# Kernel optimization log

Measured on AMD Instinct MI355X. Metric: run time of the kernel, lower is better.

## Reference

```python
import jax, jax.numpy as jnp
import numpy as np

D_MODEL = 1024
D_FF = 4096
N_HEADS = 16
D_HEAD = D_MODEL // N_HEADS
EPS = 1e-6


def setup_inputs() -> dict:
    key = jax.random.key(0)
    ks = jax.random.split(key, 12)
    B, S = 8, 1024
    s = 1.0 / np.sqrt(D_MODEL)
    inp = {
        "x": jax.random.normal(ks[0], (B, S, D_MODEL), dtype=jnp.float32),
        "mask": jnp.zeros((B, S, S), dtype=bool),
        "gamma1": jnp.ones((D_MODEL,), jnp.float32),
        "beta1": jnp.zeros((D_MODEL,), jnp.float32),
        "Wq": jax.random.normal(ks[1], (D_MODEL, D_MODEL), jnp.float32) * s,
        "bq": jnp.zeros((D_MODEL,), jnp.float32),
        "Wk": jax.random.normal(ks[2], (D_MODEL, D_MODEL), jnp.float32) * s,
        "bk": jnp.zeros((D_MODEL,), jnp.float32),
        "Wv": jax.random.normal(ks[3], (D_MODEL, D_MODEL), jnp.float32) * s,
        "bv": jnp.zeros((D_MODEL,), jnp.float32),
        "Wo": jax.random.normal(ks[4], (D_MODEL, D_MODEL), jnp.float32) * s,
        "bo": jnp.zeros((D_MODEL,), jnp.float32),
        "gamma2": jnp.ones((D_MODEL,), jnp.float32),
        "beta2": jnp.zeros((D_MODEL,), jnp.float32),
        "W1": jax.random.normal(ks[5], (D_MODEL, D_FF), jnp.float32) * s,
        "b1": jnp.zeros((D_FF,), jnp.float32),
        "W2": jax.random.normal(ks[6], (D_FF, D_MODEL), jnp.float32) * (1.0 / np.sqrt(D_FF)),
        "b2": jnp.zeros((D_MODEL,), jnp.float32),
    }
    return inp


def layer_norm(x, gamma, beta):
    mean = jnp.mean(x, axis=-1, keepdims=True)
    var = jnp.mean(jnp.square(x - mean), axis=-1, keepdims=True)  # unbiased=False
    return gamma * (x - mean) / jnp.sqrt(var + EPS) + beta


def mha(x, mask, Wq, bq, Wk, bk, Wv, bv, Wo, bo):
    B, S, _ = x.shape
    # projections: [B,S,D] -> [B,H,S,dh]
    q = (x @ Wq + bq).reshape(B, S, N_HEADS, D_HEAD).transpose(0, 2, 1, 3)
    k = (x @ Wk + bk).reshape(B, S, N_HEADS, D_HEAD).transpose(0, 2, 1, 3)
    v = (x @ Wv + bv).reshape(B, S, N_HEADS, D_HEAD).transpose(0, 2, 1, 3)
    # scores: [B,H,Sq,Sk]
    scores = jnp.einsum("bhqd,bhkd->bhqk", q, k) / np.sqrt(D_HEAD)
    scores = jnp.where(mask[:, None, :, :], -jnp.inf, scores)
    attn = jax.nn.softmax(scores, axis=-1)
    out = jnp.einsum("bhqk,bhkd->bhqd", attn, v)  # [B,H,Sq,dh]
    out = out.transpose(0, 2, 1, 3).reshape(B, S, D_MODEL)
    return out @ Wo + bo


def reference(x, mask, gamma1, beta1, Wq, bq, Wk, bk, Wv, bv, Wo, bo,
              gamma2, beta2, W1, b1, W2, b2):
    # pre-layer-norm variant per source: x = ln1(x); x = x + attn(x); x = ln2(x); x = x + ff(x)
    x = layer_norm(x, gamma1, beta1)
    x = x + mha(x, mask, Wq, bq, Wk, bk, Wv, bv, Wo, bo)
    x = layer_norm(x, gamma2, beta2)
    ff = jax.nn.relu(x @ W1 + b1) @ W2 + b2
    return x + ff
```

## Files before the change

### kernel.cpp

```cpp
#include <hip/hip_runtime.h>
#include <hip/hip_bf16.h>

typedef __bf16 bf16;
typedef __bf16 bf16x8 __attribute__((ext_vector_type(8)));
typedef __bf16 bf16x4 __attribute__((ext_vector_type(4)));
typedef float  f32x4  __attribute__((ext_vector_type(4)));

#define N_HEADS 16
#define D_HEAD  64
#define SEQ     1024
#define BATCH   8
#define MROWS   (BATCH * SEQ)

__device__ __forceinline__ void gld_lds16(const void* g, void* l) {
    __builtin_amdgcn_global_load_lds(
        (const __attribute__((address_space(1))) void*)g,
        (__attribute__((address_space(3))) void*)l, 16, 0, 0);
}

__global__ __launch_bounds__(256)
void wconv_t(const float* __restrict__ W, bf16* __restrict__ Wt, int K, int N)
{
    __shared__ float tile[32][33];
    const int tx = threadIdx.x & 31, ty = threadIdx.x >> 5;
    const int nb = blockIdx.x * 32, kb = blockIdx.y * 32;
    #pragma unroll
    for (int i = 0; i < 4; ++i)
        tile[ty + i * 8][tx] = W[(size_t)(kb + ty + i * 8) * N + nb + tx];
    __syncthreads();
    #pragma unroll
    for (int i = 0; i < 4; ++i)
        Wt[(size_t)(nb + ty + i * 8) * K + kb + tx] = (bf16)tile[tx][ty + i * 8];
}

__global__ __launch_bounds__(256)
void bconcat(const float* __restrict__ bq, const float* __restrict__ bk,
             const float* __restrict__ bv, float* __restrict__ o)
{
    const int i = blockIdx.x * 256 + threadIdx.x;
    if (i < 1024)       o[i] = bq[i];
    else if (i < 2048)  o[i] = bk[i - 1024];
    else if (i < 3072)  o[i] = bv[i - 2048];
}

__global__ __launch_bounds__(256)
void mask_pack(const unsigned char* __restrict__ m,
               unsigned long long* __restrict__ bits)
{
    const int i = blockIdx.x * 256 + threadIdx.x;
    unsigned long long b = __ballot(m[i] != 0);
    if ((threadIdx.x & 63) == 0) bits[i >> 6] = b;
}

__global__ __launch_bounds__(256)
void ln_kernel(const float* __restrict__ x, const float* __restrict__ g,
               const float* __restrict__ b, bf16* __restrict__ obf,
               float* __restrict__ of)
{
    const int row = blockIdx.x;
    const int tid = threadIdx.x;
    const float4 v = ((const float4*)(x + (size_t)row * 1024))[tid];
    float s  = v.x + v.y + v.z + v.w;
    float sq = v.x * v.x + v.y * v.y + v.z * v.z + v.w * v.w;
    #pragma unroll
    for (int off = 32; off; off >>= 1) {
        s  += __shfl_down(s, off);
        sq += __shfl_down(sq, off);
    }
    __shared__ float red[8];
    const int wid = tid >> 6, lid = tid & 63;
    if (lid == 0) { red[wid] = s; red[4 + wid] = sq; }
    __syncthreads();
    if (tid == 0) {
        float ts = red[0] + red[1] + red[2] + red[3];
        float tq = red[4] + red[5] + red[6] + red[7];
        float mean = ts * (1.f / 1024.f);
        float var  = tq * (1.f / 1024.f) - mean * mean;
        red[0] = mean;
        red[1] = rsqrtf(var + 1e-6f);
    }
    __syncthreads();
    const float mean = red[0], rstd = red[1];
    const float4 gg = ((const float4*)g)[tid];
    const float4 bb = ((const float4*)b)[tid];
    float y0 = (v.x - mean) * rstd * gg.x + bb.x;
    float y1 = (v.y - mean) * rstd * gg.y + bb.y;
    float y2 = (v.z - mean) * rstd * gg.z + bb.z;
    float y3 = (v.w - mean) * rstd * gg.w + bb.w;
    float4 o; o.x = y0; o.y = y1; o.z = y2; o.w = y3;
    ((float4*)(of + (size_t)row * 1024))[tid] = o;
    bf16x4 ob; ob[0] = (bf16)y0; ob[1] = (bf16)y1; ob[2] = (bf16)y2; ob[3] = (bf16)y3;
    ((bf16x4*)(obf + (size_t)row * 1024))[tid] = ob;
}

template <int EPI>
__global__ __launch_bounds__(256)
void gemm_bt(const bf16* __restrict__ A, const bf16* __restrict__ Bt,
             const float* __restrict__ bias, const float* __restrict__ resid,
             void* __restrict__ Cout, int M, int N, int K)
{
    __shared__ __attribute__((aligned(16))) bf16 a_lds[128 * 32];
    __shared__ __attribute__((aligned(16))) bf16 b_lds[128 * 32];
    const int tid = threadIdx.x;
    const int l = tid & 63, w = tid >> 6;
    const int lo = l & 15, hi = l >> 4;
    const int m0 = blockIdx.y * 128, n0 = blockIdx.x * 128;
    const int wrow = (w >> 1) * 64, wcol = (w & 1) * 64;
    const int srow = tid >> 2;
    const int scol = (tid & 3) * 8;

    f32x4 acc[4][4];
    #pragma unroll
    for (int i = 0; i < 4; ++i)
        #pragma unroll
        for (int j = 0; j < 4; ++j) acc[i][j] = f32x4{0.f, 0.f, 0.f, 0.f};

    const int nkt = K >> 5;
    for (int kt = 0; kt < nkt; ++kt) {
        __syncthreads();
        const bf16* ag = A  + (size_t)(m0 + srow) * K + kt * 32 + scol;
        const bf16* bg = Bt + (size_t)(n0 + srow) * K + kt * 32 + scol;
        gld_lds16(ag,                  &a_lds[srow * 32 + scol]);
        gld_lds16(ag + (size_t)64 * K, &a_lds[(64 + srow) * 32 + scol]);
        gld_lds16(bg,                  &b_lds[srow * 32 + scol]);
        gld_lds16(bg + (size_t)64 * K, &b_lds[(64 + srow) * 32 + scol]);
        asm volatile("s_waitcnt vmcnt(0)" ::: "memory");
        __syncthreads();

        bf16x8 af[4], bfr[4];
        #pragma unroll
        for (int m = 0; m < 4; ++m)
            af[m] = *(const bf16x8*)&a_lds[(wrow + m * 16 + lo) * 32 + hi * 8];
        #pragma unroll
        for (int n = 0; n < 4; ++n)
            bfr[n] = *(const bf16x8*)&b_lds[(wcol + n * 16 + lo) * 32 + hi * 8];
        #pragma unroll
        for (int m = 0; m < 4; ++m)
            #pragma unroll
            for (int n = 0; n < 4; ++n)
                acc[m][n] = __builtin_amdgcn_mfma_f32_16x16x32_bf16(af[m], bfr[n], acc[m][n], 0, 0, 0);
    }

    #pragma unroll
    for (int m = 0; m < 4; ++m) {
        const int Rbase = m0 + wrow + m * 16 + hi * 4;
        #pragma unroll
        for (int n = 0; n < 4; ++n) {
            const int Cc = n0 + wcol + n * 16 + lo;
            const float bv = bias[Cc];
            #pragma unroll
            for (int r = 0; r < 4; ++r) {
                const int Rr = Rbase + r;
                float vv = acc[m][n][r] + bv;
                if (EPI == 0) {
                    const int b_ = Rr >> 10, s_ = Rr & 1023;
                    const int which = Cc >> 10;
                    const int cc = Cc & 1023;
                    const int h_ = cc >> 6, d_ = cc & 63;
                    ((bf16*)Cout)[(size_t)which * ((size_t)MROWS * 1024) +
                                  (((size_t)(b_ * 16 + h_) * 1024 + s_) << 6) + d_] = (bf16)vv;
                } else if (EPI == 1) {
                    vv += resid[(size_t)Rr * N + Cc];
                    ((float*)Cout)[(size_t)Rr * N + Cc] = vv;
                } else {
                    vv = fmaxf(vv, 0.f);
                    ((bf16*)Cout)[(size_t)Rr * N + Cc] = (bf16)vv;
                }
            }
        }
    }
}

__global__ __launch_bounds__(256)
void attn_kernel(const bf16* __restrict__ q, const bf16* __restrict__ k,
                 const bf16* __restrict__ v,
                 const unsigned long long* __restrict__ mbits,
                 bf16* __restrict__ ctx)
{
    __shared__ __attribute__((aligned(16))) bf16 q_lds[64][72];
    __shared__ __attribute__((aligned(16))) bf16 k_lds[64][72];
    __shared__ __attribute__((aligned(16))) bf16 vt_lds[64][72];
    __shared__ __attribute__((aligned(16))) bf16 p_lds[4][16][72];

    const int id = blockIdx.x;
    const int swz = (id & 7) * 256 + (id >> 3);
    const int qt = swz & 15;
    const int bh = swz >> 4;
    const int hh = bh & 15, bb = bh >> 4;
    const int tid = threadIdx.x;
    const int w = tid >> 6, l = tid & 63;
    const int lo = l & 15, hi = l >> 4;

    {
        const bf16* qg = q + ((size_t)bh * SEQ + qt * 64) * D_HEAD;
        #pragma unroll
        for (int i = 0; i < 2; ++i) {
            const int e = (i * 256 + tid) * 8;
            const int r = e >> 6, c = e & 63;
            *(uint4*)&q_lds[r][c] = *(const uint4*)(qg + r * 64 + c);
        }
    }

    f32x4 oacc[4];
    float m_r[4], l_r[4];
    #pragma unroll
    for (int i = 0; i < 4; ++i) {
        oacc[i] = f32x4{0.f, 0.f, 0.f, 0.f};
        m_r[i] = -__builtin_inff();
        l_r[i] = 0.f;
    }

    for (int kt = 0; kt < 16; ++kt) {
        __syncthreads();
        const bf16* kg = k + ((size_t)bh * SEQ + kt * 64) * D_HEAD;
        const bf16* vg = v + ((size_t)bh * SEQ + kt * 64) * D_HEAD;
        #pragma unroll
        for (int i = 0; i < 2; ++i) {
            const int e = (i * 256 + tid) * 8;
            const int r = e >> 6, c = e & 63;
            *(uint4*)&k_lds[r][c] = *(const uint4*)(kg + r * 64 + c);
            uint4 tv = *(const uint4*)(vg + r * 64 + c);
            const bf16* pv = (const bf16*)&tv;
            const int colS = r ^ (((c >> 3) & 7) << 3);
            #pragma unroll
            for (int j = 0; j < 8; ++j) vt_lds[c + j][colS] = pv[j];
        }
        unsigned long long mb[4];
        #pragma unroll
        for (int r = 0; r < 4; ++r) {
            const int qrow = qt * 64 + w * 16 + hi * 4 + r;
            mb[r] = mbits[((((size_t)bb << 10) | qrow) << 4) + kt];
        }
        __syncthreads();

        f32x4 sf[4];
        #pragma unroll
        for (int ct = 0; ct < 4; ++ct) {
            f32x4 sa = f32x4{0.f, 0.f, 0.f, 0.f};
            #pragma unroll
            for (int kk = 0; kk < 2; ++kk) {
                bf16x8 a   = *(const bf16x8*)&q_lds[w * 16 + lo][kk * 32 + hi * 8];
                bf16x8 bfr = *(const bf16x8*)&k_lds[ct * 16 + lo][kk * 32 + hi * 8];
                sa = __builtin_amdgcn_mfma_f32_16x16x32_bf16(a, bfr, sa, 0, 0, 0);
            }
            sf[ct] = sa;
        }

        float pm[4];
        #pragma unroll
        for (int r = 0; r < 4; ++r) {
            #pragma unroll
            for (int ct = 0; ct < 4; ++ct) {
                float sv = sf[ct][r] * 0.125f;
                if ((mb[r] >> (ct * 16 + lo)) & 1ull) sv = -__builtin_inff();
                sf[ct][r] = sv;
            }
            float t0 = fmaxf(fmaxf(sf[0][r], sf[1][r]), fmaxf(sf[2][r], sf[3][r]));
            #pragma unroll
            for (int off = 1; off < 16; off <<= 1) t0 = fmaxf(t0, __shfl_xor(t0, off));
            pm[r] = t0;
        }
        float scl[4];
        #pragma unroll
        for (int r = 0; r < 4; ++r) {
            const float mn = fmaxf(m_r[r], pm[r]);
            scl[r] = __expf(m_r[r] - mn);
            m_r[r] = mn;
            float acc_s = 0.f;
            #pragma unroll
            for (int ct = 0; ct < 4; ++ct) {
                const float p = __expf(sf[ct][r] - mn);
                sf[ct][r] = p;
                acc_s += p;
            }
            #pragma unroll
            for (int off = 1; off < 16; off <<= 1) acc_s += __shfl_xor(acc_s, off);
            l_r[r] = l_r[r] * scl[r] + acc_s;
        }
        #pragma unroll
        for (int n = 0; n < 4; ++n)
            #pragma unroll
            for (int r = 0; r < 4; ++r) oacc[n][r] *= scl[r];

        #pragma unroll
        for (int ct = 0; ct < 4; ++ct)
            #pragma unroll
            for (int r = 0; r < 4; ++r)
                p_lds[w][hi * 4 + r][ct * 16 + lo] = (bf16)sf[ct][r];
        asm volatile("s_waitcnt lgkmcnt(0)" ::: "memory");

        #pragma unroll
        for (int n = 0; n < 4; ++n) {
            const int g = (((n * 16 + lo) >> 3) & 7) << 3;
            #pragma unroll
            for (int kk = 0; kk < 2; ++kk) {
                bf16x8 a   = *(const bf16x8*)&p_lds[w][lo][kk * 32 + hi * 8];
                bf16x8 bfr = *(const bf16x8*)&vt_lds[n * 16 + lo][(kk * 32 + hi * 8) ^ g];
                oacc[n] = __builtin_amdgcn_mfma_f32_16x16x32_bf16(a, bfr, oacc[n], 0, 0, 0);
            }
        }
    }

    #pragma unroll
    for (int r = 0; r < 4; ++r) {
        const float inv = 1.f / l_r[r];
        const size_t srow = (size_t)bb * SEQ + qt * 64 + w * 16 + hi * 4 + r;
        const size_t base = (srow * N_HEADS + hh) * D_HEAD;
        #pragma unroll
        for (int n = 0; n < 4; ++n)
            ctx[base + n * 16 + lo] = (bf16)(oacc[n][r] * inv);
    }
}

extern "C" void kernel_launch(void* const* d_in, const int* in_sizes, int n_in,
                              void* d_out, int out_size, void* d_ws, size_t ws_size,
                              hipStream_t stream)
{
    const float* x      = (const float*)d_in[0];
    const unsigned char* mask = (const unsigned char*)d_in[1];
    const float* gamma1 = (const float*)d_in[2];
    const float* beta1  = (const float*)d_in[3];
    const float* Wq     = (const float*)d_in[4];
    const float* bq     = (const float*)d_in[5];
    const float* Wk     = (const float*)d_in[6];
    const float* bk     = (const float*)d_in[7];
    const float* Wv     = (const float*)d_in[8];
    const float* bv     = (const float*)d_in[9];
    const float* Wo     = (const float*)d_in[10];
    const float* bo     = (const float*)d_in[11];
    const float* gamma2 = (const float*)d_in[12];
    const float* beta2  = (const float*)d_in[13];
    const float* W1     = (const float*)d_in[14];
    const float* b1     = (const float*)d_in[15];
    const float* W2     = (const float*)d_in[16];
    const float* b2     = (const float*)d_in[17];

    char* ws = (char*)d_ws;
    const size_t MB = 1u << 20;
    bf16* wqkv = (bf16*)(ws + 0 * MB);
    bf16* wot  = (bf16*)(ws + 6 * MB);
    bf16* w1t  = (bf16*)(ws + 8 * MB);
    bf16* w2t  = (bf16*)(ws + 16 * MB);
    unsigned long long* mbits = (unsigned long long*)(ws + 16 * MB);
    float* bqkv = (float*)(ws + 17 * MB);
    bf16* xn1b = (bf16*)(ws + 24 * MB);
    float* xn1f = (float*)(ws + 40 * MB);
    bf16* qkv  = (bf16*)(ws + 72 * MB);
    bf16* ctx  = (bf16*)(ws + 120 * MB);
    bf16* hbuf = (bf16*)(ws + 72 * MB);
    bf16* xn2b = (bf16*)(ws + 136 * MB);
    float* xn2f = (float*)(ws + 152 * MB);
    float* x2f = (float*)d_out;

    wconv_t<<<dim3(32, 32),  256, 0, stream>>>(Wq, wqkv,               1024, 1024);
    wconv_t<<<dim3(32, 32),  256, 0, stream>>>(Wk, wqkv + 1024 * 1024, 1024, 1024);
    wconv_t<<<dim3(32, 32),  256, 0, stream>>>(Wv, wqkv + 2048 * 1024, 1024, 1024);
    wconv_t<<<dim3(32, 32),  256, 0, stream>>>(Wo, wot, 1024, 1024);
    wconv_t<<<dim3(128, 32), 256, 0, stream>>>(W1, w1t, 1024, 4096);
    bconcat<<<12, 256, 0, stream>>>(bq, bk, bv, bqkv);
    mask_pack<<<32768, 256, 0, stream>>>(mask, mbits);

    ln_kernel<<<MROWS, 256, 0, stream>>>(x, gamma1, beta1, xn1b, xn1f);

    gemm_bt<0><<<dim3(24, 64), 256, 0, stream>>>(xn1b, wqkv, bqkv, nullptr, qkv, MROWS, 3072, 1024);

    attn_kernel<<<2048, 256, 0, stream>>>(qkv, qkv + (size_t)MROWS * 1024,
                                          qkv + (size_t)2 * MROWS * 1024, mbits, ctx);

    wconv_t<<<dim3(32, 128), 256, 0, stream>>>(W2, w2t, 4096, 1024);

    gemm_bt<1><<<dim3(8, 64), 256, 0, stream>>>(ctx, wot, bo, xn1f, x2f, MROWS, 1024, 1024);

    ln_kernel<<<MROWS, 256, 0, stream>>>(x2f, gamma2, beta2, xn2b, xn2f);

    gemm_bt<2><<<dim3(32, 64), 256, 0, stream>>>(xn2b, w1t, b1, nullptr, hbuf, MROWS, 4096, 1024);

    gemm_bt<1><<<dim3(8, 64), 256, 0, stream>>>(hbuf, w2t, b2, xn2f, (float*)d_out, MROWS, 1024, 4096);
}
```

Baseline: 661.0 us.

## Double GEMM K-tile, XOR-swizzle LDS, and remap blocks across XCDs

The bf16 GEMM now stages a 64-wide K slice per iteration instead of 32, which halves the number of barrier and wait round-trips per output tile. LDS rows are XOR-swizzled in 16-byte chunks to avoid bank conflicts on the fragment reads. Block IDs are linearised and remapped so that consecutive tiles land on the same XCD (8-way interleave), which should improve L2 reuse. LDS usage per block doubles to 32 KB, which could limit occupancy, and the remap assumes the grid size is divisible by 8.

```diff
diff --git a/kernel.cpp b/kernel.cpp
--- a/kernel.cpp
+++ b/kernel.cpp
@@ -97,17 +97,23 @@
 __global__ __launch_bounds__(256)
 void gemm_bt(const bf16* __restrict__ A, const bf16* __restrict__ Bt,
              const float* __restrict__ bias, const float* __restrict__ resid,
-             void* __restrict__ Cout, int M, int N, int K)
-{
-    __shared__ __attribute__((aligned(16))) bf16 a_lds[128 * 32];
-    __shared__ __attribute__((aligned(16))) bf16 b_lds[128 * 32];
+             void* __restrict__ Cout, int M, int N, int K, int nbx)
+{
+    __shared__ __attribute__((aligned(16))) bf16 a_lds[128 * 64];
+    __shared__ __attribute__((aligned(16))) bf16 b_lds[128 * 64];
     const int tid = threadIdx.x;
     const int l = tid & 63, w = tid >> 6;
     const int lo = l & 15, hi = l >> 4;
-    const int m0 = blockIdx.y * 128, n0 = blockIdx.x * 128;
+
+    const int nwg = gridDim.x;
+    const int nid = (blockIdx.x & 7) * (nwg >> 3) + (blockIdx.x >> 3);
+    const int bx = nid % nbx, by = nid / nbx;
+    const int m0 = by * 128, n0 = bx * 128;
+
     const int wrow = (w >> 1) * 64, wcol = (w & 1) * 64;
-    const int srow = tid >> 2;
-    const int scol = (tid & 3) * 8;
+    const int srow = tid >> 3;
+    const int c8   = tid & 7;
+    const int c8g  = c8 ^ (srow & 7);
 
     f32x4 acc[4][4];
     #pragma unroll
@@ -115,30 +121,40 @@
         #pragma unroll
         for (int j = 0; j < 4; ++j) acc[i][j] = f32x4{0.f, 0.f, 0.f, 0.f};
 
-    const int nkt = K >> 5;
+    const int nkt = K >> 6;
     for (int kt = 0; kt < nkt; ++kt) {
         __syncthreads();
-        const bf16* ag = A  + (size_t)(m0 + srow) * K + kt * 32 + scol;
-        const bf16* bg = Bt + (size_t)(n0 + srow) * K + kt * 32 + scol;
-        gld_lds16(ag,                  &a_lds[srow * 32 + scol]);
-        gld_lds16(ag + (size_t)64 * K, &a_lds[(64 + srow) * 32 + scol]);
-        gld_lds16(bg,                  &b_lds[srow * 32 + scol]);
-        gld_lds16(bg + (size_t)64 * K, &b_lds[(64 + srow) * 32 + scol]);
+        const int kc = kt * 64 + c8g * 8;
+        #pragma unroll
+        for (int blk = 0; blk < 4; ++blk) {
+            const int row = blk * 32 + srow;
+            gld_lds16(A  + (size_t)(m0 + row) * K + kc, &a_lds[row * 64 + c8 * 8]);
+            gld_lds16(Bt + (size_t)(n0 + row) * K + kc, &b_lds[row * 64 + c8 * 8]);
+        }
         asm volatile("s_waitcnt vmcnt(0)" ::: "memory");
         __syncthreads();
 
-        bf16x8 af[4], bfr[4];
-        #pragma unroll
-        for (int m = 0; m < 4; ++m)
-            af[m] = *(const bf16x8*)&a_lds[(wrow + m * 16 + lo) * 32 + hi * 8];
-        #pragma unroll
-        for (int n = 0; n < 4; ++n)
-            bfr[n] = *(const bf16x8*)&b_lds[(wcol + n * 16 + lo) * 32 + hi * 8];
-        #pragma unroll
-        for (int m = 0; m < 4; ++m)
-            #pragma unroll
-            for (int n = 0; n < 4; ++n)
-                acc[m][n] = __builtin_amdgcn_mfma_f32_16x16x32_bf16(af[m], bfr[n], acc[m][n], 0, 0, 0);
+        #pragma unroll
+        for (int kk2 = 0; kk2 < 2; ++kk2) {
+            bf16x8 af[4], bfr[4];
+            #pragma unroll
+            for (int m = 0; m < 4; ++m) {
+                const int row = wrow + m * 16 + lo;
+                const int ch = ((kk2 * 4 + hi) ^ (lo & 7)) << 3;
+                af[m] = *(const bf16x8*)&a_lds[row * 64 + ch];
+            }
+            #pragma unroll
+            for (int n = 0; n < 4; ++n) {
+                const int row = wcol + n * 16 + lo;
+                const int ch = ((kk2 * 4 + hi) ^ (lo & 7)) << 3;
+                bfr[n] = *(const bf16x8*)&b_lds[row * 64 + ch];
+            }
+            #pragma unroll
+            for (int m = 0; m < 4; ++m)
+                #pragma unroll
+                for (int n = 0; n < 4; ++n)
+                    acc[m][n] = __builtin_amdgcn_mfma_f32_16x16x32_bf16(af[m], bfr[n], acc[m][n], 0, 0, 0);
+        }
     }
 
     #pragma unroll
@@ -362,18 +378,18 @@
 
     ln_kernel<<<MROWS, 256, 0, stream>>>(x, gamma1, beta1, xn1b, xn1f);
 
-    gemm_bt<0><<<dim3(24, 64), 256, 0, stream>>>(xn1b, wqkv, bqkv, nullptr, qkv, MROWS, 3072, 1024);
+    gemm_bt<0><<<24 * 64, 256, 0, stream>>>(xn1b, wqkv, bqkv, nullptr, qkv, MROWS, 3072, 1024, 24);
 
     attn_kernel<<<2048, 256, 0, stream>>>(qkv, qkv + (size_t)MROWS * 1024,
                                           qkv + (size_t)2 * MROWS * 1024, mbits, ctx);
 
     wconv_t<<<dim3(32, 128), 256, 0, stream>>>(W2, w2t, 4096, 1024);
 
-    gemm_bt<1><<<dim3(8, 64), 256, 0, stream>>>(ctx, wot, bo, xn1f, x2f, MROWS, 1024, 1024);
+    gemm_bt<1><<<8 * 64, 256, 0, stream>>>(ctx, wot, bo, xn1f, x2f, MROWS, 1024, 1024, 8);
 
     ln_kernel<<<MROWS, 256, 0, stream>>>(x2f, gamma2, beta2, xn2b, xn2f);
 
-    gemm_bt<2><<<dim3(32, 64), 256, 0, stream>>>(xn2b, w1t, b1, nullptr, hbuf, MROWS, 4096, 1024);
-
-    gemm_bt<1><<<dim3(8, 64), 256, 0, stream>>>(hbuf, w2t, b2, xn2f, (float*)d_out, MROWS, 1024, 4096);
-}
+    gemm_bt<2><<<32 * 64, 256, 0, stream>>>(xn2b, w1t, b1, nullptr, hbuf, MROWS, 4096, 1024, 32);
+
+    gemm_bt<1><<<8 * 64, 256, 0, stream>>>(hbuf, w2t, b2, xn2f, (float*)d_out, MROWS, 1024, 4096, 8);
+}
```

Result: faster. 634.1 us (-4.1%).
